# Kernel optimization log

Measured on AMD Instinct MI355X. Metric: run time of the kernel, lower is better.

Reference implementation:

```python
import jax, jax.numpy as jnp
import numpy as np

D_MODEL = 1024
NHEAD = 16
HEAD_DIM = D_MODEL // NHEAD
B, S = 4, 2048
LN_EPS = 1e-5


def setup_inputs() -> dict:
    key = jax.random.key(0)
    ks = jax.random.split(key, 16)
    def lin(k, fin, fout):
        # torch nn.Linear default init scale ~ 1/sqrt(fin)
        s = 1.0 / np.sqrt(fin)
        kw, kb = jax.random.split(k)
        W = jax.random.uniform(kw, (fin, fout), jnp.float32, -s, s)
        b = jax.random.uniform(kb, (fout,), jnp.float32, -s, s)
        return W, b
    Wq, bq = lin(ks[0], D_MODEL, D_MODEL)
    Wk, bk = lin(ks[1], D_MODEL, D_MODEL)
    Wv, bv = lin(ks[2], D_MODEL, D_MODEL)
    Wo, bo = lin(ks[3], D_MODEL, D_MODEL)
    W1, b1 = lin(ks[4], D_MODEL, 2 * D_MODEL)
    W2, b2 = lin(ks[5], 2 * D_MODEL, D_MODEL)
    return {
        "query": jax.random.normal(ks[6], (B, S, D_MODEL), jnp.float32),
        "key": jax.random.normal(ks[7], (B, S, D_MODEL), jnp.float32),
        "value": jax.random.normal(ks[8], (B, S, D_MODEL), jnp.float32),
        "mask": jnp.ones((1, 1, S, S), dtype=bool),
        "Wq": Wq, "bq": bq, "Wk": Wk, "bk": bk, "Wv": Wv, "bv": bv,
        "Wo": Wo, "bo": bo,
        "ln_g": jnp.ones((D_MODEL,), jnp.float32),
        "ln_b": jnp.zeros((D_MODEL,), jnp.float32),
        "W1": W1, "b1": b1, "W2": W2, "b2": b2,
    }


def _layer_norm(x, g, b):
    mu = jnp.mean(x, axis=-1, keepdims=True)
    var = jnp.mean(jnp.square(x - mu), axis=-1, keepdims=True)
    return (x - mu) * jax.lax.rsqrt(var + LN_EPS) * g + b


def reference(query, key, value, mask, Wq, bq, Wk, bk, Wv, bv, Wo, bo,
              ln_g, ln_b, W1, b1, W2, b2):
    Bq, Sq, _ = query.shape
    # projections -> [B, H, S, hd]
    def split_heads(x):
        return x.reshape(Bq, -1, NHEAD, HEAD_DIM).transpose(0, 2, 1, 3)
    q = split_heads(query @ Wq + bq)
    k = split_heads(key @ Wk + bk)
    v = split_heads(value @ Wv + bv)
    scores = jnp.einsum("bhqd,bhkd->bhqk", q, k) / jnp.sqrt(
        jnp.asarray(HEAD_DIM, q.dtype))
    scores = jnp.where(mask, scores, jnp.asarray(-jnp.inf, scores.dtype))
    probs = jax.nn.softmax(scores, axis=-1)  # dropout is identity at eval
    ctx = jnp.einsum("bhqk,bhkd->bhqd", probs, v)
    ctx = ctx.transpose(0, 2, 1, 3).reshape(Bq, Sq, D_MODEL)
    out = ctx @ Wo + bo
    # residual with (pre-projection) query input, then layer norm
    out = _layer_norm(query + out, ln_g, ln_b)
    # FFN: Linear -> ReLU -> Linear
    out = jax.nn.relu(out @ W1 + b1) @ W2 + b2
    return out
```

## Files before the change

kernel.cpp:

```cpp
#include <hip/hip_runtime.h>

typedef unsigned short u16;
typedef u16 u16x4 __attribute__((ext_vector_type(4)));
typedef u16 u16x8 __attribute__((ext_vector_type(8)));
typedef __bf16 bf16x8 __attribute__((ext_vector_type(8)));
typedef float f32x4 __attribute__((ext_vector_type(4)));

__device__ __forceinline__ u16 f2bf(float f) {
  return __builtin_bit_cast(u16, (__bf16)f);
}

__device__ __forceinline__ bf16x8 ldbf8(const u16* p) {
  union { u16x8 u; bf16x8 b; } t;
  t.u = *(const u16x8*)p;
  return t.b;
}

__device__ __forceinline__ bf16x8 cat44(u16x4 a, u16x4 b) {
  union { u16x4 h[2]; bf16x8 v; } t;
  t.h[0] = a; t.h[1] = b;
  return t.v;
}

typedef __attribute__((address_space(3))) u16 lds_u16;
typedef __attribute__((address_space(1))) const u16 glb_u16;

__device__ __forceinline__ void async16(const u16* g, u16* l) {
  __builtin_amdgcn_global_load_lds((glb_u16*)g, (lds_u16*)l, 16, 0, 0);
}

#if __has_builtin(__builtin_amdgcn_exp2f)
#define EXP2(x) __builtin_amdgcn_exp2f(x)
#else
#define EXP2(x) exp2f(x)
#endif

struct PrepDesc { const float* W; u16* WT; int K; int N; };
struct Prep { PrepDesc d[6]; const float* cs[3]; u16* cd[3]; };

__global__ __launch_bounds__(256, 4) void prep_k(Prep p) {
  const int z = blockIdx.z;
  if (z < 6) {
    PrepDesc dd = p.d[z];
    const int n0 = blockIdx.x * 32, k0 = blockIdx.y * 32;
    if (n0 >= dd.N || k0 >= dd.K) return;
    __shared__ float tt[32][33];
    const int tx = threadIdx.x & 31, ty = threadIdx.x >> 5;
#pragma unroll
    for (int i = 0; i < 4; i++) {
      int k = ty + i * 8;
      tt[k][tx] = dd.W[(size_t)(k0 + k) * dd.N + n0 + tx];
    }
    __syncthreads();
#pragma unroll
    for (int i = 0; i < 4; i++) {
      int n = ty + i * 8;
      dd.WT[(size_t)(n0 + n) * dd.K + k0 + tx] = f2bf(tt[tx][n]);
    }
  } else {
    const float* src = p.cs[z - 6];
    u16* dst = p.cd[z - 6];
    size_t base = ((size_t)(blockIdx.y * 64 + blockIdx.x)) * 2048 + threadIdx.x * 4;
#pragma unroll
    for (int j = 0; j < 2; j++) {
      f32x4 v = *(const f32x4*)(src + base + j * 1024);
      u16x4 o;
      o.x = f2bf(v.x); o.y = f2bf(v.y); o.z = f2bf(v.z); o.w = f2bf(v.w);
      *(u16x4*)(dst + base + j * 1024) = o;
    }
  }
}

__global__ __launch_bounds__(256, 3) void qkv_k(const u16* __restrict__ qb,
                                                const u16* __restrict__ kb,
                                                const u16* __restrict__ vb,
                                                const u16* __restrict__ WqT,
                                                const u16* __restrict__ WkT,
                                                const u16* __restrict__ WvT,
                                                const float* __restrict__ bq,
                                                const float* __restrict__ bk,
                                                const float* __restrict__ bv,
                                                u16* __restrict__ qp,
                                                u16* __restrict__ kp,
                                                u16* __restrict__ vp) {
  const int tid = threadIdx.x;
  const int lane = tid & 63, w = tid >> 6;
  const int c = lane & 15, quad = lane >> 4;
  const int z = blockIdx.z, bx = blockIdx.x, by = blockIdx.y;
  int n0, m0;
  const u16 *A, *B;
  if (z < 2) {
    n0 = (bx & 7) * 128; m0 = (by * 8 + (bx >> 3)) * 128;
    A = z ? kb : qb; B = z ? WkT : WqT;
  } else {
    n0 = bx * 128; m0 = by * 128;
    A = WvT; B = vb;
  }
  const int wm = (w >> 1) * 64, wn = (w & 1) * 64;

  __shared__ u16 sA[128 * 64];
  __shared__ u16 sB[128 * 64];

  f32x4 acc[4][4];
#pragma unroll
  for (int mi = 0; mi < 4; mi++)
#pragma unroll
    for (int ni = 0; ni < 4; ni++) acc[mi][ni] = 0.f;

  for (int k0 = 0; k0 < 1024; k0 += 64) {
    __syncthreads();
#pragma unroll
    for (int cb = 0; cb < 4; cb++) {
      int fl = w * 4 + cb;
      int row = fl * 8 + (lane >> 3), col = (lane & 7) * 8;
      async16(B + (size_t)(n0 + row) * 1024 + k0 + col, &sB[fl * 512]);
      async16(A + (size_t)(m0 + row) * 1024 + k0 + col, &sA[fl * 512]);
    }
    __syncthreads();

#pragma unroll
    for (int ks = 0; ks < 2; ks++) {
      bf16x8 af[4], bg[4];
#pragma unroll
      for (int mi = 0; mi < 4; mi++)
        af[mi] = ldbf8(&sA[(wm + mi * 16 + c) * 64 + ks * 32 + quad * 8]);
#pragma unroll
      for (int ni = 0; ni < 4; ni++)
        bg[ni] = ldbf8(&sB[(wn + ni * 16 + c) * 64 + ks * 32 + quad * 8]);
#pragma unroll
      for (int mi = 0; mi < 4; mi++)
#pragma unroll
        for (int ni = 0; ni < 4; ni++)
          acc[mi][ni] = __builtin_amdgcn_mfma_f32_16x16x32_bf16(af[mi], bg[ni], acc[mi][ni], 0, 0, 0);
    }
  }

#pragma unroll
  for (int mi = 0; mi < 4; mi++)
#pragma unroll
    for (int ni = 0; ni < 4; ni++)
#pragma unroll
      for (int r = 0; r < 4; r++) {
        int row = m0 + wm + mi * 16 + quad * 4 + r;
        int col = n0 + wn + ni * 16 + c;
        if (z < 2) {
          const float* bias = z ? bk : bq;
          u16* out = z ? kp : qp;
          float v = acc[mi][ni][r] + bias[col];
          int b = row >> 11, s = row & 2047, h = col >> 6, d = col & 63;
          out[(((size_t)(b * 16 + h) * 2048 + s) << 6) + d] = f2bf(v);
        } else {
          float v = acc[mi][ni][r] + bv[row];
          int b = col >> 11, s = col & 2047, h = row >> 6, d = row & 63;
          vp[(((size_t)(b * 16 + h) * 64 + d) << 11) + s] = f2bf(v);
        }
      }
}

template <int MODE>
__global__ __launch_bounds__(256, 3) void gemm128_k(const u16* __restrict__ A,
                                                    const u16* __restrict__ B,
                                                    const float* __restrict__ bias,
                                                    const float* __restrict__ resid,
                                                    void* __restrict__ Out,
                                                    int M, int N, int K) {
  const int tid = threadIdx.x;
  const int lane = tid & 63, w = tid >> 6;
  const int c = lane & 15, quad = lane >> 4;
  const int n0 = blockIdx.x * 128, m0 = blockIdx.y * 128;
  const int wm = (w >> 1) * 64, wn = (w & 1) * 64;

  __shared__ u16 sA[128 * 64];
  __shared__ u16 sB[128 * 64];

  f32x4 acc[4][4];
#pragma unroll
  for (int mi = 0; mi < 4; mi++)
#pragma unroll
    for (int ni = 0; ni < 4; ni++) acc[mi][ni] = 0.f;

  for (int k0 = 0; k0 < K; k0 += 64) {
    __syncthreads();
#pragma unroll
    for (int cb = 0; cb < 4; cb++) {
      int fl = w * 4 + cb;
      int row = fl * 8 + (lane >> 3), col = (lane & 7) * 8;
      async16(B + (size_t)(n0 + row) * K + k0 + col, &sB[fl * 512]);
      async16(A + (size_t)(m0 + row) * K + k0 + col, &sA[fl * 512]);
    }
    __syncthreads();

#pragma unroll
    for (int ks = 0; ks < 2; ks++) {
      bf16x8 af[4], bg[4];
#pragma unroll
      for (int mi = 0; mi < 4; mi++)
        af[mi] = ldbf8(&sA[(wm + mi * 16 + c) * 64 + ks * 32 + quad * 8]);
#pragma unroll
      for (int ni = 0; ni < 4; ni++)
        bg[ni] = ldbf8(&sB[(wn + ni * 16 + c) * 64 + ks * 32 + quad * 8]);
#pragma unroll
      for (int mi = 0; mi < 4; mi++)
#pragma unroll
        for (int ni = 0; ni < 4; ni++)
          acc[mi][ni] = __builtin_amdgcn_mfma_f32_16x16x32_bf16(af[mi], bg[ni], acc[mi][ni], 0, 0, 0);
    }
  }

#pragma unroll
  for (int mi = 0; mi < 4; mi++)
#pragma unroll
    for (int ni = 0; ni < 4; ni++)
#pragma unroll
      for (int r = 0; r < 4; r++) {
        int row = m0 + wm + mi * 16 + quad * 4 + r;
        int col = n0 + wn + ni * 16 + c;
        float v = acc[mi][ni][r] + bias[col];
        if constexpr (MODE == 1) {
          v += resid[(size_t)row * N + col];
          ((float*)Out)[(size_t)row * N + col] = v;
        } else if constexpr (MODE == 2) {
          v = fmaxf(v, 0.f);
          ((u16*)Out)[(size_t)row * N + col] = f2bf(v);
        } else {
          ((float*)Out)[(size_t)row * N + col] = v;
        }
      }
}

__global__ __launch_bounds__(256, 4) void attn_k(const u16* __restrict__ Qp,
                                                 const u16* __restrict__ Kp,
                                                 const u16* __restrict__ Vt,
                                                 u16* __restrict__ ctx) {
  const int tid = threadIdx.x, lane = tid & 63, w = tid >> 6;
  const int c = lane & 15, quad = lane >> 4;
  const int bh = blockIdx.x, qt = blockIdx.y;
  const int b = bh >> 4, h = bh & 15;

  __shared__ u16 lds[2 * 64 * 72];
  u16* Kt = lds;
  u16* Vs = lds + 64 * 72;

  const u16* Qb = Qp + ((size_t)bh * 2048 + qt * 128 + w * 32) * 64;
  bf16x8 aq[2][2];
#pragma unroll
  for (int st = 0; st < 2; st++)
#pragma unroll
    for (int ks = 0; ks < 2; ks++)
      aq[st][ks] = ldbf8(Qb + (st * 16 + c) * 64 + ks * 32 + quad * 8);

  const float SC = 0.18033688011112042f;
  f32x4 o[2][4];
  float rs[2] = {0.f, 0.f};
#pragma unroll
  for (int st = 0; st < 2; st++)
#pragma unroll
    for (int dt = 0; dt < 4; dt++) o[st][dt] = 0.f;

  const u16* Kb0 = Kp + (size_t)bh * 2048 * 64;
  const u16* Vb0 = Vt + (size_t)bh * 64 * 2048;
  const int sr = tid >> 3, sc8 = (tid & 7) * 8;

  u16x8 kr[2], vr[2];
#pragma unroll
  for (int j = 0; j < 2; j++) {
    kr[j] = *(const u16x8*)(Kb0 + ((size_t)(j * 32 + sr)) * 64 + sc8);
    vr[j] = *(const u16x8*)(Vb0 + (size_t)(j * 32 + sr) * 2048 + sc8);
  }

  for (int kt = 0; kt < 32; kt++) {
    __syncthreads();
#pragma unroll
    for (int j = 0; j < 2; j++) {
      *(u16x8*)&Kt[(j * 32 + sr) * 72 + sc8] = kr[j];
      *(u16x8*)&Vs[(j * 32 + sr) * 72 + sc8] = vr[j];
    }
    __syncthreads();
    if (kt < 31) {
#pragma unroll
      for (int j = 0; j < 2; j++) {
        kr[j] = *(const u16x8*)(Kb0 + ((size_t)(kt + 1) * 64 + j * 32 + sr) * 64 + sc8);
        vr[j] = *(const u16x8*)(Vb0 + (size_t)(j * 32 + sr) * 2048 + (kt + 1) * 64 + sc8);
      }
    }

    f32x4 sT[2][4];
#pragma unroll
    for (int ct = 0; ct < 4; ct++) {
      bf16x8 ka0 = ldbf8(&Kt[(ct * 16 + c) * 72 + 0 + quad * 8]);
      bf16x8 ka1 = ldbf8(&Kt[(ct * 16 + c) * 72 + 32 + quad * 8]);
#pragma unroll
      for (int st = 0; st < 2; st++) {
        f32x4 t = 0.f;
        t = __builtin_amdgcn_mfma_f32_16x16x32_bf16(ka0, aq[st][0], t, 0, 0, 0);
        t = __builtin_amdgcn_mfma_f32_16x16x32_bf16(ka1, aq[st][1], t, 0, 0, 0);
        sT[st][ct] = t;
      }
    }

    u16x4 pb[2][4];
#pragma unroll
    for (int st = 0; st < 2; st++)
#pragma unroll
      for (int ct = 0; ct < 4; ct++)
#pragma unroll
        for (int r = 0; r < 4; r++) {
          float pf = EXP2(sT[st][ct][r] * SC);
          rs[st] += pf;
          pb[st][ct][r] = f2bf(pf);
        }

#pragma unroll
    for (int kh = 0; kh < 2; kh++) {
      bf16x8 pB[2];
#pragma unroll
      for (int st = 0; st < 2; st++) pB[st] = cat44(pb[st][2 * kh], pb[st][2 * kh + 1]);
#pragma unroll
      for (int dt = 0; dt < 4; dt++) {
        const u16* vrow = &Vs[(dt * 16 + c) * 72 + kh * 32 + quad * 4];
        bf16x8 A8 = cat44(*(const u16x4*)vrow, *(const u16x4*)(vrow + 16));
#pragma unroll
        for (int st = 0; st < 2; st++)
          o[st][dt] = __builtin_amdgcn_mfma_f32_16x16x32_bf16(A8, pB[st], o[st][dt], 0, 0, 0);
      }
    }
  }

  float inv[2];
#pragma unroll
  for (int st = 0; st < 2; st++) {
    float r = rs[st];
    r += __shfl_xor(r, 16);
    r += __shfl_xor(r, 32);
    inv[st] = 1.0f / r;
  }

  __syncthreads();
  u16* Ob = lds + w * 2304;
#pragma unroll
  for (int st = 0; st < 2; st++)
#pragma unroll
    for (int dt = 0; dt < 4; dt++)
#pragma unroll
      for (int r = 0; r < 4; r++)
        Ob[(st * 16 + c) * 72 + dt * 16 + quad * 4 + r] = f2bf(o[st][dt][r] * inv[st]);
#pragma unroll
  for (int j = 0; j < 4; j++) {
    int r_ = j * 8 + (lane >> 3), dc = (lane & 7) * 8;
    u16x8 v = *(const u16x8*)&Ob[r_ * 72 + dc];
    int s_ = qt * 128 + w * 32 + r_;
    *(u16x8*)&ctx[((size_t)b * 2048 + s_) * 1024 + h * 64 + dc] = v;
  }
}

__global__ __launch_bounds__(256, 4) void ln_k(const float* __restrict__ X,
                                               const float* __restrict__ g,
                                               const float* __restrict__ bt,
                                               u16* __restrict__ out) {
  const int row = blockIdx.x, tid = threadIdx.x;
  const float* x = X + (size_t)row * 1024;
  f32x4 v = *(const f32x4*)(x + tid * 4);
  float s = v.x + v.y + v.z + v.w;
  float sq = v.x * v.x + v.y * v.y + v.z * v.z + v.w * v.w;
#pragma unroll
  for (int off = 1; off < 64; off <<= 1) {
    s += __shfl_xor(s, off);
    sq += __shfl_xor(sq, off);
  }
  __shared__ float red[4][2];
  if ((tid & 63) == 0) { red[tid >> 6][0] = s; red[tid >> 6][1] = sq; }
  __syncthreads();
  s = red[0][0] + red[1][0] + red[2][0] + red[3][0];
  sq = red[0][1] + red[1][1] + red[2][1] + red[3][1];
  float mu = s * (1.0f / 1024.0f);
  float var = sq * (1.0f / 1024.0f) - mu * mu;
  float rstd = rsqrtf(var + 1e-5f);
#pragma unroll
  for (int j = 0; j < 4; j++) {
    int col = tid * 4 + j;
    out[(size_t)row * 1024 + col] = f2bf((v[j] - mu) * rstd * g[col] + bt[col]);
  }
}

extern "C" void kernel_launch(void* const* d_in, const int* in_sizes, int n_in,
                              void* d_out, int out_size, void* d_ws, size_t ws_size,
                              hipStream_t stream) {
  const float* query = (const float*)d_in[0];
  const float* key_  = (const float*)d_in[1];
  const float* value = (const float*)d_in[2];
  const float* Wq = (const float*)d_in[4];  const float* bq = (const float*)d_in[5];
  const float* Wk = (const float*)d_in[6];  const float* bk = (const float*)d_in[7];
  const float* Wv = (const float*)d_in[8];  const float* bv = (const float*)d_in[9];
  const float* Wo = (const float*)d_in[10]; const float* bo = (const float*)d_in[11];
  const float* ln_g = (const float*)d_in[12]; const float* ln_b = (const float*)d_in[13];
  const float* W1 = (const float*)d_in[14]; const float* b1 = (const float*)d_in[15];
  const float* W2 = (const float*)d_in[16]; const float* b2 = (const float*)d_in[17];

  const size_t MB = 1u << 20;
  if (ws_size < 112 * MB) return;
  char* ws = (char*)d_ws;
  u16* WqT = (u16*)(ws + 0 * MB);
  u16* WkT = (u16*)(ws + 2 * MB);
  u16* WvT = (u16*)(ws + 4 * MB);
  u16* WoT = (u16*)(ws + 6 * MB);
  u16* W1T = (u16*)(ws + 8 * MB);
  u16* W2T = (u16*)(ws + 12 * MB);
  u16* qb  = (u16*)(ws + 16 * MB);
  u16* kb  = (u16*)(ws + 32 * MB);
  u16* vb  = (u16*)(ws + 48 * MB);
  u16* qp  = (u16*)(ws + 64 * MB);
  u16* kp  = (u16*)(ws + 80 * MB);
  u16* vp  = (u16*)(ws + 96 * MB);
  u16* ctxp = (u16*)(ws + 16 * MB);
  float* resid = (float*)(ws + 32 * MB);
  u16* xb = (u16*)(ws + 64 * MB);
  u16* hb = (u16*)(ws + 80 * MB);

  Prep p;
  p.d[0] = {Wq, WqT, 1024, 1024}; p.d[1] = {Wk, WkT, 1024, 1024};
  p.d[2] = {Wv, WvT, 1024, 1024}; p.d[3] = {Wo, WoT, 1024, 1024};
  p.d[4] = {W1, W1T, 1024, 2048}; p.d[5] = {W2, W2T, 2048, 1024};
  p.cs[0] = query; p.cs[1] = key_; p.cs[2] = value;
  p.cd[0] = qb;    p.cd[1] = kb;   p.cd[2] = vb;
  prep_k<<<dim3(64, 64, 9), 256, 0, stream>>>(p);

  qkv_k<<<dim3(64, 8, 3), 256, 0, stream>>>(qb, kb, vb, WqT, WkT, WvT,
                                            bq, bk, bv, qp, kp, vp);

  attn_k<<<dim3(64, 16), 256, 0, stream>>>(qp, kp, vp, ctxp);

  gemm128_k<1><<<dim3(8, 64), 256, 0, stream>>>(ctxp, WoT, bo, query, resid, 8192, 1024, 1024);

  ln_k<<<8192, 256, 0, stream>>>(resid, ln_g, ln_b, xb);

  gemm128_k<2><<<dim3(16, 64), 256, 0, stream>>>(xb, W1T, b1, nullptr, hb, 8192, 2048, 1024);
  gemm128_k<3><<<dim3(8, 64), 256, 0, stream>>>(hb, W2T, b2, nullptr, (float*)d_out, 8192, 1024, 2048);
}
```

Measured before the change: 496.3 us.

## Register-prefetch GEMM tiles with padded LDS rows instead of direct global-to-LDS loads

Replaces the direct global_load_lds staging in the QKV and generic GEMM kernels with a shared core that prefetches the next K tile into registers while MFMAs run on the current tile. The LDS row stride is padded from 64 to 72 elements to reduce bank conflicts on fragment reads. This is meant to overlap global memory latency with compute and speed up LDS reads. In exchange it uses more VGPRs for the prefetch buffers, which could reduce occupancy, and it adds an extra register-to-LDS store pass.

```diff
diff --git a/kernel.cpp b/kernel.cpp
--- a/kernel.cpp
+++ b/kernel.cpp
@@ -20,13 +20,6 @@
   union { u16x4 h[2]; bf16x8 v; } t;
   t.h[0] = a; t.h[1] = b;
   return t.v;
-}
-
-typedef __attribute__((address_space(3))) u16 lds_u16;
-typedef __attribute__((address_space(1))) const u16 glb_u16;
-
-__device__ __forceinline__ void async16(const u16* g, u16* l) {
-  __builtin_amdgcn_global_load_lds((glb_u16*)g, (lds_u16*)l, 16, 0, 0);
 }
 
 #if __has_builtin(__builtin_amdgcn_exp2f)
@@ -67,6 +60,65 @@
       u16x4 o;
       o.x = f2bf(v.x); o.y = f2bf(v.y); o.z = f2bf(v.z); o.w = f2bf(v.w);
       *(u16x4*)(dst + base + j * 1024) = o;
+    }
+  }
+}
+
+struct Acc44 { f32x4 a[4][4]; };
+
+__device__ __forceinline__ void gemm_core(const u16* __restrict__ A,
+                                          const u16* __restrict__ B,
+                                          int m0, int n0, int K,
+                                          int tid, int wm, int wn, int c, int quad,
+                                          u16* sA, u16* sB, Acc44& acc) {
+#pragma unroll
+  for (int mi = 0; mi < 4; mi++)
+#pragma unroll
+    for (int ni = 0; ni < 4; ni++) acc.a[mi][ni] = 0.f;
+
+  const int sr = tid >> 3, sc8 = (tid & 7) * 8;
+  const u16* Ap = A + (size_t)(m0 + sr) * K + sc8;
+  const u16* Bp = B + (size_t)(n0 + sr) * K + sc8;
+
+  u16x8 ar[4], br[4];
+#pragma unroll
+  for (int j = 0; j < 4; j++) {
+    ar[j] = *(const u16x8*)(Ap + (size_t)(j * 32) * K);
+    br[j] = *(const u16x8*)(Bp + (size_t)(j * 32) * K);
+  }
+
+  const int kIters = K >> 6;
+  for (int kt = 0; kt < kIters; kt++) {
+    __syncthreads();
+#pragma unroll
+    for (int j = 0; j < 4; j++) {
+      *(u16x8*)&sA[(j * 32 + sr) * 72 + sc8] = ar[j];
+      *(u16x8*)&sB[(j * 32 + sr) * 72 + sc8] = br[j];
+    }
+    __syncthreads();
+    if (kt + 1 < kIters) {
+      const u16* Ap2 = Ap + (kt + 1) * 64;
+      const u16* Bp2 = Bp + (kt + 1) * 64;
+#pragma unroll
+      for (int j = 0; j < 4; j++) {
+        ar[j] = *(const u16x8*)(Ap2 + (size_t)(j * 32) * K);
+        br[j] = *(const u16x8*)(Bp2 + (size_t)(j * 32) * K);
+      }
+    }
+#pragma unroll
+    for (int ks = 0; ks < 2; ks++) {
+      bf16x8 af[4], bg[4];
+#pragma unroll
+      for (int mi = 0; mi < 4; mi++)
+        af[mi] = ldbf8(&sA[(wm + mi * 16 + c) * 72 + ks * 32 + quad * 8]);
+#pragma unroll
+      for (int ni = 0; ni < 4; ni++)
+        bg[ni] = ldbf8(&sB[(wn + ni * 16 + c) * 72 + ks * 32 + quad * 8]);
+#pragma unroll
+      for (int mi = 0; mi < 4; mi++)
+#pragma unroll
+        for (int ni = 0; ni < 4; ni++)
+          acc.a[mi][ni] = __builtin_amdgcn_mfma_f32_16x16x32_bf16(af[mi], bg[ni], acc.a[mi][ni], 0, 0, 0);
     }
   }
 }
@@ -98,42 +150,10 @@
   }
   const int wm = (w >> 1) * 64, wn = (w & 1) * 64;
 
-  __shared__ u16 sA[128 * 64];
-  __shared__ u16 sB[128 * 64];
-
-  f32x4 acc[4][4];
-#pragma unroll
-  for (int mi = 0; mi < 4; mi++)
-#pragma unroll
-    for (int ni = 0; ni < 4; ni++) acc[mi][ni] = 0.f;
-
-  for (int k0 = 0; k0 < 1024; k0 += 64) {
-    __syncthreads();
-#pragma unroll
-    for (int cb = 0; cb < 4; cb++) {
-      int fl = w * 4 + cb;
-      int row = fl * 8 + (lane >> 3), col = (lane & 7) * 8;
-      async16(B + (size_t)(n0 + row) * 1024 + k0 + col, &sB[fl * 512]);
-      async16(A + (size_t)(m0 + row) * 1024 + k0 + col, &sA[fl * 512]);
-    }
-    __syncthreads();
-
-#pragma unroll
-    for (int ks = 0; ks < 2; ks++) {
-      bf16x8 af[4], bg[4];
-#pragma unroll
-      for (int mi = 0; mi < 4; mi++)
-        af[mi] = ldbf8(&sA[(wm + mi * 16 + c) * 64 + ks * 32 + quad * 8]);
-#pragma unroll
-      for (int ni = 0; ni < 4; ni++)
-        bg[ni] = ldbf8(&sB[(wn + ni * 16 + c) * 64 + ks * 32 + quad * 8]);
-#pragma unroll
-      for (int mi = 0; mi < 4; mi++)
-#pragma unroll
-        for (int ni = 0; ni < 4; ni++)
-          acc[mi][ni] = __builtin_amdgcn_mfma_f32_16x16x32_bf16(af[mi], bg[ni], acc[mi][ni], 0, 0, 0);
-    }
-  }
+  __shared__ u16 sA[128 * 72];
+  __shared__ u16 sB[128 * 72];
+  Acc44 acc;
+  gemm_core(A, B, m0, n0, 1024, tid, wm, wn, c, quad, sA, sB, acc);
 
 #pragma unroll
   for (int mi = 0; mi < 4; mi++)
@@ -146,11 +166,11 @@
         if (z < 2) {
           const float* bias = z ? bk : bq;
           u16* out = z ? kp : qp;
-          float v = acc[mi][ni][r] + bias[col];
+          float v = acc.a[mi][ni][r] + bias[col];
           int b = row >> 11, s = row & 2047, h = col >> 6, d = col & 63;
           out[(((size_t)(b * 16 + h) * 2048 + s) << 6) + d] = f2bf(v);
         } else {
-          float v = acc[mi][ni][r] + bv[row];
+          float v = acc.a[mi][ni][r] + bv[row];
           int b = col >> 11, s = col & 2047, h = row >> 6, d = row & 63;
           vp[(((size_t)(b * 16 + h) * 64 + d) << 11) + s] = f2bf(v);
         }
@@ -170,42 +190,10 @@
   const int n0 = blockIdx.x * 128, m0 = blockIdx.y * 128;
   const int wm = (w >> 1) * 64, wn = (w & 1) * 64;
 
-  __shared__ u16 sA[128 * 64];
-  __shared__ u16 sB[128 * 64];
-
-  f32x4 acc[4][4];
-#pragma unroll
-  for (int mi = 0; mi < 4; mi++)
-#pragma unroll
-    for (int ni = 0; ni < 4; ni++) acc[mi][ni] = 0.f;
-
-  for (int k0 = 0; k0 < K; k0 += 64) {
-    __syncthreads();
-#pragma unroll
-    for (int cb = 0; cb < 4; cb++) {
-      int fl = w * 4 + cb;
-      int row = fl * 8 + (lane >> 3), col = (lane & 7) * 8;
-      async16(B + (size_t)(n0 + row) * K + k0 + col, &sB[fl * 512]);
-      async16(A + (size_t)(m0 + row) * K + k0 + col, &sA[fl * 512]);
-    }
-    __syncthreads();
-
-#pragma unroll
-    for (int ks = 0; ks < 2; ks++) {
-      bf16x8 af[4], bg[4];
-#pragma unroll
-      for (int mi = 0; mi < 4; mi++)
-        af[mi] = ldbf8(&sA[(wm + mi * 16 + c) * 64 + ks * 32 + quad * 8]);
-#pragma unroll
-      for (int ni = 0; ni < 4; ni++)
-        bg[ni] = ldbf8(&sB[(wn + ni * 16 + c) * 64 + ks * 32 + quad * 8]);
-#pragma unroll
-      for (int mi = 0; mi < 4; mi++)
-#pragma unroll
-        for (int ni = 0; ni < 4; ni++)
-          acc[mi][ni] = __builtin_amdgcn_mfma_f32_16x16x32_bf16(af[mi], bg[ni], acc[mi][ni], 0, 0, 0);
-    }
-  }
+  __shared__ u16 sA[128 * 72];
+  __shared__ u16 sB[128 * 72];
+  Acc44 acc;
+  gemm_core(A, B, m0, n0, K, tid, wm, wn, c, quad, sA, sB, acc);
 
 #pragma unroll
   for (int mi = 0; mi < 4; mi++)
@@ -215,7 +203,7 @@
       for (int r = 0; r < 4; r++) {
         int row = m0 + wm + mi * 16 + quad * 4 + r;
         int col = n0 + wn + ni * 16 + c;
-        float v = acc[mi][ni][r] + bias[col];
+        float v = acc.a[mi][ni][r] + bias[col];
         if constexpr (MODE == 1) {
           v += resid[(size_t)row * N + col];
           ((float*)Out)[(size_t)row * N + col] = v;
```

Measured after the change: 482.3 us. 2.8% less time.
